# Kernel tuning notes

Hardware: AMD Instinct MI355X
Metric: run time of the kernel (lower is better)

Reference implementation:

```python
import jax, jax.numpy as jnp
import numpy as np

VOCAB, D_MODEL, N_EXPERTS, TOP_K = 32000, 768, 8, 2
D_FF = 4 * D_MODEL
BATCH, SEQ = 2, 2048


def setup_inputs() -> dict:
    key = jax.random.key(0)
    ks = jax.random.split(key, 6)
    s = 0.02
    return {
        "x": jax.random.randint(ks[0], (BATCH, SEQ), 0, VOCAB),
        "emb": jax.random.normal(ks[1], (VOCAB, D_MODEL), jnp.float32) * s,
        "gate_w": jax.random.normal(ks[2], (D_MODEL, N_EXPERTS), jnp.float32) * s,
        "gate_b": jnp.zeros((N_EXPERTS,), jnp.float32),
        "exp_w": jax.random.normal(ks[3], (N_EXPERTS, D_MODEL, D_FF), jnp.float32) * s,
        "exp_b": jnp.zeros((N_EXPERTS, D_FF), jnp.float32),
        "head_w": jax.random.normal(ks[4], (D_FF, VOCAB), jnp.float32) * s,
        "head_b": jnp.zeros((VOCAB,), jnp.float32),
    }


def reference(x, emb, gate_w, gate_b, exp_w, exp_b, head_w, head_b):
    B, S = x.shape
    h = emb[x]                                   # [B,S,D] embedding gather
    t = h.reshape(B * S, -1)                     # [T,D] token view
    logits = t @ gate_w + gate_b                 # [T,E] router
    topv, topi = jax.lax.top_k(logits, TOP_K)    # top-2 routing
    w = jax.nn.softmax(topv, axis=-1)            # renormalized gate weights
    T = t.shape[0]
    gates = jnp.zeros_like(logits).at[jnp.arange(T)[:, None], topi].set(w)  # [T,E]
    # expert FFN: Linear(d_model -> 4*d_model) + ReLU, dense over experts
    exp_out = jax.nn.relu(jnp.einsum('td,edf->tef', t, exp_w) + exp_b)      # [T,E,F]
    moe = jnp.einsum('te,tef->tf', gates, exp_out)                          # combine
    out = moe @ head_w + head_b                  # [T,V]
    return out.reshape(B, S, -1)
```

## Files before the change

### kernel.cpp

```cpp
#include <hip/hip_runtime.h>

typedef unsigned short u16;
typedef __attribute__((ext_vector_type(8))) short short8;
typedef __attribute__((ext_vector_type(4))) float f32x4;

#define T_TOKENS 4096
#define DMODEL   768
#define DFF      3072
#define NEXP     8
#define NVOCAB   32000

__device__ __forceinline__ u16 f2bf(float f) {
  unsigned u = __float_as_uint(f);
  u += 0x7FFFu + ((u >> 16) & 1u);
  return (u16)(u >> 16);
}
__device__ __forceinline__ float bf2f(u16 b) {
  return __uint_as_float(((unsigned)b) << 16);
}

__device__ __forceinline__ void async_load16(const void* g, void* lds) {
  __builtin_amdgcn_global_load_lds((const __attribute__((address_space(1))) void*)g,
                                   (__attribute__((address_space(3))) void*)lds, 16, 0, 0);
}

#define SBAR() __builtin_amdgcn_s_barrier()
#define VMCNT(n) asm volatile("s_waitcnt vmcnt(" #n ")")
#define SCHEDB() __builtin_amdgcn_sched_barrier(0)

__global__ __launch_bounds__(256) void k_embed_router(
    const int* __restrict__ x, const float* __restrict__ emb,
    const float* __restrict__ gw, const float* __restrict__ gb,
    u16* __restrict__ tbf, int* __restrict__ counts,
    int* __restrict__ tlist, float* __restrict__ wlist)
{
  __shared__ float partial[4][NEXP];
  const int t = blockIdx.x;
  const int tok = x[t];
  const float* er = emb + (size_t)tok * DMODEL;
  float p[NEXP];
#pragma unroll
  for (int e = 0; e < NEXP; ++e) p[e] = 0.f;
#pragma unroll
  for (int i = 0; i < 3; ++i) {
    const int d = threadIdx.x + i * 256;
    const float v = er[d];
    tbf[(size_t)t * DMODEL + d] = f2bf(v);
#pragma unroll
    for (int e = 0; e < NEXP; ++e) p[e] += v * gw[d * NEXP + e];
  }
#pragma unroll
  for (int e = 0; e < NEXP; ++e)
#pragma unroll
    for (int m = 32; m >= 1; m >>= 1) p[e] += __shfl_xor(p[e], m);
  const int lane = threadIdx.x & 63, wv = threadIdx.x >> 6;
  if (lane == 0)
    for (int e = 0; e < NEXP; ++e) partial[wv][e] = p[e];
  __syncthreads();
  if (threadIdx.x == 0) {
    float l[NEXP];
    for (int e = 0; e < NEXP; ++e)
      l[e] = partial[0][e] + partial[1][e] + partial[2][e] + partial[3][e] + gb[e];
    int i0 = 0;
    for (int e = 1; e < NEXP; ++e) if (l[e] > l[i0]) i0 = e;
    int i1 = -1;
    for (int e = 0; e < NEXP; ++e) { if (e == i0) continue; if (i1 < 0 || l[e] > l[i1]) i1 = e; }
    const float w0 = 1.f / (1.f + expf(l[i1] - l[i0]));
    int p0 = atomicAdd(&counts[0 * NEXP + i0], 1);
    tlist[(0 * NEXP + i0) * T_TOKENS + p0] = t;
    wlist[(0 * NEXP + i0) * T_TOKENS + p0] = w0;
    int p1 = atomicAdd(&counts[1 * NEXP + i1], 1);
    tlist[(1 * NEXP + i1) * T_TOKENS + p1] = t;
    wlist[(1 * NEXP + i1) * T_TOKENS + p1] = 1.f - w0;
  }
}

__global__ __launch_bounds__(256) void k_transpose_cvt(
    const float* __restrict__ src, u16* __restrict__ dst, int R, int C)
{
  __shared__ float tile[32][33];
  const float* s = src + (size_t)blockIdx.z * R * C;
  u16* d = dst + (size_t)blockIdx.z * R * C;
  const int tx = threadIdx.x & 31, ty = threadIdx.x >> 5;
  const int c = blockIdx.x * 32 + tx;
#pragma unroll
  for (int i = 0; i < 4; ++i) {
    const int r = blockIdx.y * 32 + ty + i * 8;
    tile[ty + i * 8][tx] = s[(size_t)r * C + c];
  }
  __syncthreads();
  const int rr = blockIdx.y * 32 + tx;
#pragma unroll
  for (int i = 0; i < 4; ++i) {
    const int cc = blockIdx.x * 32 + ty + i * 8;
    d[(size_t)cc * R + rr] = f2bf(tile[tx][ty + i * 8]);
  }
}

template <int SLOT1>
__global__ __launch_bounds__(256) void k_ffn_slot(
    const u16* __restrict__ tbf, const u16* __restrict__ BT,
    const float* __restrict__ eb, const int* __restrict__ counts,
    const int* __restrict__ tlist, const float* __restrict__ wlist,
    u16* __restrict__ moe)
{
  const int e = blockIdx.z;
  const int cnt = counts[SLOT1 * NEXP + e];
  const int mb = blockIdx.y;
  if (mb * 128 >= cnt) return;
  const int base = (SLOT1 * NEXP + e) * T_TOKENS + mb * 128;
  const int lim = cnt - mb * 128;

  __shared__ u16 aT[128 * 64];
  __shared__ u16 bT[128 * 64];
  const int tid = threadIdx.x;
  const int wave = tid >> 6, lane = tid & 63;
  const int wm = wave >> 1, wn = wave & 1;
  const int kg = lane >> 4, fr = lane & 15;
  const int n0 = blockIdx.x * 128;
  const u16* Be = BT + (size_t)e * DFF * DMODEL;

  int tokm[4];
#pragma unroll
  for (int it = 0; it < 4; ++it) {
    const int m = (it * 256 + tid) >> 3;
    tokm[it] = tlist[base + (m < lim ? m : lim - 1)];
  }

  f32x4 acc[4][4] = {};
  for (int ks = 0; ks < DMODEL / 64; ++ks) {
    __syncthreads();
    const int kb = ks * 64;
#pragma unroll
    for (int it = 0; it < 4; ++it) {
      const int c = it * 256 + tid;
      const int m = c >> 3;
      const int slot = (c & 7) ^ (m & 7);
      async_load16(tbf + (size_t)tokm[it] * DMODEL + kb + slot * 8,
                   &aT[(it * 256 + wave * 64) * 8]);
      async_load16(Be + (size_t)(n0 + m) * DMODEL + kb + slot * 8,
                   &bT[(it * 256 + wave * 64) * 8]);
    }
    __syncthreads();
#pragma unroll
    for (int kk = 0; kk < 2; ++kk) {
      short8 af[4], bf[4];
#pragma unroll
      for (int i = 0; i < 4; ++i) {
        const int am = wm * 64 + i * 16 + fr;
        const int kc = kk * 4 + kg;
        af[i] = *(const short8*)&aT[(am * 8 + (kc ^ (am & 7))) * 8];
        const int bn = wn * 64 + i * 16 + fr;
        bf[i] = *(const short8*)&bT[(bn * 8 + (kc ^ (bn & 7))) * 8];
      }
#pragma unroll
      for (int i = 0; i < 4; ++i)
#pragma unroll
        for (int j = 0; j < 4; ++j)
          acc[i][j] = __builtin_amdgcn_mfma_f32_16x16x32_bf16(af[i], bf[j], acc[i][j], 0, 0, 0);
    }
  }

  int trow[4][4]; float wrow[4][4];
#pragma unroll
  for (int i = 0; i < 4; ++i)
#pragma unroll
    for (int r = 0; r < 4; ++r) {
      const int row = wm * 64 + i * 16 + kg * 4 + r;
      if (row < lim) { trow[i][r] = tlist[base + row]; wrow[i][r] = wlist[base + row]; }
      else trow[i][r] = -1;
    }
#pragma unroll
  for (int j = 0; j < 4; ++j) {
    const int col = n0 + wn * 64 + j * 16 + fr;
    const float b = eb[e * DFF + col];
#pragma unroll
    for (int i = 0; i < 4; ++i)
#pragma unroll
      for (int r = 0; r < 4; ++r) {
        if (trow[i][r] < 0) continue;
        float v = acc[i][j][r] + b;
        v = v > 0.f ? v : 0.f;
        v *= wrow[i][r];
        u16* dst = &moe[(size_t)trow[i][r] * DFF + col];
        if (SLOT1) v += bf2f(*dst);
        *dst = f2bf(v);
      }
  }
}

__device__ __forceinline__ short8 frag(const u16* buf, int row, int kc) {
  return *(const short8*)(buf + (row * 8 + (kc ^ (row & 7))) * 8);
}

__global__ __launch_bounds__(512, 2) void k_head(
    const u16* __restrict__ A, const u16* __restrict__ BT,
    const float* __restrict__ bias, float* __restrict__ C)
{
  __shared__ u16 aL[2][256 * 64];
  __shared__ u16 bL[2][256 * 64];
  const int tid = threadIdx.x;
  const int lane = tid & 63, wave = tid >> 6;
  const int wm = wave >> 2, wn = wave & 3;
  const int kg = lane >> 4, fr = lane & 15;
  const int wg = (int)blockIdx.x;
  const int swz = (wg & 7) * 250 + (wg >> 3);
  const int m0 = (swz & 15) * 256;
  const int n0 = (swz >> 4) * 256;
  const int K = DFF, NT = K / 64;

  size_t gAo[2], gBo[2]; int lAo[2], lBo[2];
#pragma unroll
  for (int i = 0; i < 2; ++i) {
    const int c = i * 512 + tid, rl = c >> 3, s = c & 7;
    const int rA = (rl & 63) + ((rl >> 6) << 7);
    const int gsA = s ^ (rA & 7);
    gAo[i] = (size_t)(m0 + rA) * K + gsA * 8;
    lAo[i] = rA * 64 + s * 8;
    const int rB = (rl & 31) + ((rl >> 5) << 6);
    const int gsB = s ^ (rB & 7);
    gBo[i] = (size_t)(n0 + rB) * K + gsB * 8;
    lBo[i] = rB * 64 + s * 8;
  }
  auto stageA = [&](int kb, u16* buf, int h) {
#pragma unroll
    for (int i = 0; i < 2; ++i)
      async_load16(A + gAo[i] + (size_t)(h * 64) * K + kb, buf + lAo[i] + h * 4096);
  };
  auto stageB = [&](int kb, u16* buf, int h) {
#pragma unroll
    for (int i = 0; i < 2; ++i)
      async_load16(BT + gBo[i] + (size_t)(h * 32) * K + kb, buf + lBo[i] + h * 2048);
  };

  f32x4 acc[8][4] = {};
  short8 af[4][2], bfl[2][2], bfh[2][2];

  stageA(0, aL[0], 0); stageA(0, aL[0], 1);
  stageB(0, bL[0], 0); stageB(0, bL[0], 1);
  stageA(64, aL[1], 0); stageB(64, bL[1], 0); stageB(64, bL[1], 1);
  VMCNT(6);
  SCHEDB();
  SBAR();
#pragma unroll
  for (int mi = 0; mi < 4; ++mi)
#pragma unroll
    for (int kk = 0; kk < 2; ++kk)
      af[mi][kk] = frag(aL[0], wm * 128 + mi * 16 + fr, kk * 4 + kg);
#pragma unroll
  for (int ni = 0; ni < 2; ++ni)
#pragma unroll
    for (int kk = 0; kk < 2; ++kk) {
      bfl[ni][kk] = frag(bL[0], wn * 64 + ni * 16 + fr, kk * 4 + kg);
      bfh[ni][kk] = frag(bL[0], wn * 64 + 32 + ni * 16 + fr, kk * 4 + kg);
    }

  for (int t = 0; t < NT; ++t) {
    const int cur = t & 1;
    const u16* a_ = aL[cur];
    const u16* b_ = bL[cur];
    u16* aw = aL[cur];
    u16* bw = bL[cur];
    u16* an = aL[cur ^ 1];
    const u16* bn = bL[cur ^ 1];
    const int kb1 = (t + 1) * 64, kb2 = (t + 2) * 64;

    if (t + 1 < NT) stageA(kb1, an, 1);
    __builtin_amdgcn_s_setprio(1);
#pragma unroll
    for (int mi = 0; mi < 4; ++mi)
#pragma unroll
      for (int ni = 0; ni < 2; ++ni)
#pragma unroll
        for (int kk = 0; kk < 2; ++kk) {
          acc[mi][ni]     = __builtin_amdgcn_mfma_f32_16x16x32_bf16(af[mi][kk], bfl[ni][kk], acc[mi][ni], 0, 0, 0);
          acc[mi][ni + 2] = __builtin_amdgcn_mfma_f32_16x16x32_bf16(af[mi][kk], bfh[ni][kk], acc[mi][ni + 2], 0, 0, 0);
        }
    __builtin_amdgcn_s_setprio(0);
#pragma unroll
    for (int mi = 0; mi < 4; ++mi)
#pragma unroll
      for (int kk = 0; kk < 2; ++kk)
        af[mi][kk] = frag(a_, wm * 128 + 64 + mi * 16 + fr, kk * 4 + kg);
    if (t + 1 < NT) { VMCNT(2); SCHEDB(); }
    SBAR();

    if (t + 2 < NT) { stageA(kb2, aw, 0); stageB(kb2, bw, 0); stageB(kb2, bw, 1); }
    __builtin_amdgcn_s_setprio(1);
#pragma unroll
    for (int mi = 0; mi < 4; ++mi)
#pragma unroll
      for (int ni = 0; ni < 2; ++ni)
#pragma unroll
        for (int kk = 0; kk < 2; ++kk) {
          acc[mi + 4][ni]     = __builtin_amdgcn_mfma_f32_16x16x32_bf16(af[mi][kk], bfl[ni][kk], acc[mi + 4][ni], 0, 0, 0);
          acc[mi + 4][ni + 2] = __builtin_amdgcn_mfma_f32_16x16x32_bf16(af[mi][kk], bfh[ni][kk], acc[mi + 4][ni + 2], 0, 0, 0);
        }
    __builtin_amdgcn_s_setprio(0);
    if (t + 1 < NT) {
#pragma unroll
      for (int mi = 0; mi < 4; ++mi)
#pragma unroll
        for (int kk = 0; kk < 2; ++kk)
          af[mi][kk] = frag(an, wm * 128 + mi * 16 + fr, kk * 4 + kg);
#pragma unroll
      for (int ni = 0; ni < 2; ++ni)
#pragma unroll
        for (int kk = 0; kk < 2; ++kk) {
          bfl[ni][kk] = frag(bn, wn * 64 + ni * 16 + fr, kk * 4 + kg);
          bfh[ni][kk] = frag(bn, wn * 64 + 32 + ni * 16 + fr, kk * 4 + kg);
        }
      if (t + 2 < NT) { VMCNT(6); } else { VMCNT(0); }
      SCHEDB();
    }
    SBAR();
  }

#pragma unroll
  for (int ni = 0; ni < 4; ++ni) {
    const int col = n0 + wn * 64 + ni * 16 + fr;
    const float b = bias[col];
#pragma unroll
    for (int mi = 0; mi < 8; ++mi) {
      const int row = m0 + wm * 128 + (mi >> 2) * 64 + (mi & 3) * 16 + kg * 4;
#pragma unroll
      for (int r = 0; r < 4; ++r)
        __builtin_nontemporal_store(acc[mi][ni][r] + b,
                                    &C[(size_t)(row + r) * NVOCAB + col]);
    }
  }
}

extern "C" void kernel_launch(void* const* d_in, const int* in_sizes, int n_in,
                              void* d_out, int out_size, void* d_ws, size_t ws_size,
                              hipStream_t stream) {
  const int*   x     = (const int*)d_in[0];
  const float* emb   = (const float*)d_in[1];
  const float* gw    = (const float*)d_in[2];
  const float* gb    = (const float*)d_in[3];
  const float* expw  = (const float*)d_in[4];
  const float* expb  = (const float*)d_in[5];
  const float* headw = (const float*)d_in[6];
  const float* headb = (const float*)d_in[7];
  float* out = (float*)d_out;

  char* ws = (char*)d_ws;
  size_t off = 0;
  auto alloc = [&](size_t bytes) { size_t r = off; off += (bytes + 255) & ~(size_t)255; return r; };
  u16*   tbf    = (u16*)(ws + alloc((size_t)T_TOKENS * DMODEL * 2));
  int*   counts = (int*)(ws + alloc(2 * NEXP * 4));
  int*   tlist  = (int*)(ws + alloc((size_t)2 * NEXP * T_TOKENS * 4));
  float* wlist  = (float*)(ws + alloc((size_t)2 * NEXP * T_TOKENS * 4));
  u16*   expwT  = (u16*)(ws + alloc((size_t)NEXP * DFF * DMODEL * 2));
  u16*   headwT = (u16*)(ws + alloc((size_t)NVOCAB * DFF * 2));
  u16*   moe    = (u16*)(ws + alloc((size_t)T_TOKENS * DFF * 2));

  hipMemsetAsync(counts, 0, 2 * NEXP * 4, stream);
  k_embed_router<<<T_TOKENS, 256, 0, stream>>>(x, emb, gw, gb, tbf, counts, tlist, wlist);
  k_transpose_cvt<<<dim3(DFF / 32, DMODEL / 32, NEXP), 256, 0, stream>>>(expw, expwT, DMODEL, DFF);
  k_transpose_cvt<<<dim3(NVOCAB / 32, DFF / 32, 1), 256, 0, stream>>>(headw, headwT, DFF, NVOCAB);
  k_ffn_slot<0><<<dim3(DFF / 128, T_TOKENS / 128, NEXP), 256, 0, stream>>>(
      tbf, expwT, expb, counts, tlist, wlist, moe);
  k_ffn_slot<1><<<dim3(DFF / 128, T_TOKENS / 128, NEXP), 256, 0, stream>>>(
      tbf, expwT, expb, counts, tlist, wlist, moe);
  k_head<<<(T_TOKENS / 256) * (NVOCAB / 256), 512, 0, stream>>>(moe, headwT, headb, out);
}
```

Baseline: 1.181 ms.

## Double-buffer FFN expert GEMM with async prefetch and widen transpose tiles

The expert FFN kernel now double-buffers its LDS tiles and stages the next K-slices with async global-to-LDS loads while MFMAs run on the current slice. Fragment reads are split into halves and synchronisation is done with explicit vmcnt waits and barriers, replacing the two full syncthreads per K step. The weight transpose-convert kernel moves to 64x64 tiles and writes two bf16 values per 32-bit store. In exchange the FFN kernel uses twice the LDS and has a harder wait/barrier schedule to reason about.

Result: no change. 1.167 ms, median of 2 (-1.2%).

```diff
diff --git a/kernel.cpp b/kernel.cpp
--- a/kernel.cpp
+++ b/kernel.cpp
@@ -27,6 +27,10 @@
 #define SBAR() __builtin_amdgcn_s_barrier()
 #define VMCNT(n) asm volatile("s_waitcnt vmcnt(" #n ")")
 #define SCHEDB() __builtin_amdgcn_sched_barrier(0)
+
+__device__ __forceinline__ short8 frag(const u16* buf, int row, int kc) {
+  return *(const short8*)(buf + (row * 8 + (kc ^ (row & 7))) * 8);
+}
 
 __global__ __launch_bounds__(256) void k_embed_router(
     const int* __restrict__ x, const float* __restrict__ emb,
@@ -78,22 +82,26 @@
 __global__ __launch_bounds__(256) void k_transpose_cvt(
     const float* __restrict__ src, u16* __restrict__ dst, int R, int C)
 {
-  __shared__ float tile[32][33];
+  __shared__ float tile[64][65];
   const float* s = src + (size_t)blockIdx.z * R * C;
   u16* d = dst + (size_t)blockIdx.z * R * C;
-  const int tx = threadIdx.x & 31, ty = threadIdx.x >> 5;
-  const int c = blockIdx.x * 32 + tx;
-#pragma unroll
-  for (int i = 0; i < 4; ++i) {
-    const int r = blockIdx.y * 32 + ty + i * 8;
-    tile[ty + i * 8][tx] = s[(size_t)r * C + c];
+  const int tx = threadIdx.x & 63, ty = threadIdx.x >> 6;
+  const int c = blockIdx.x * 64 + tx;
+#pragma unroll
+  for (int i = 0; i < 16; ++i) {
+    const int r = blockIdx.y * 64 + ty + i * 4;
+    tile[ty + i * 4][tx] = s[(size_t)r * C + c];
   }
   __syncthreads();
-  const int rr = blockIdx.y * 32 + tx;
-#pragma unroll
-  for (int i = 0; i < 4; ++i) {
-    const int cc = blockIdx.x * 32 + ty + i * 8;
-    d[(size_t)cc * R + rr] = f2bf(tile[tx][ty + i * 8]);
+  const int h = threadIdx.x & 31, v = threadIdx.x >> 5;
+  const int rr = blockIdx.y * 64 + h * 2;
+#pragma unroll
+  for (int i = 0; i < 8; ++i) {
+    const int ccl = v + i * 8;
+    const int cc = blockIdx.x * 64 + ccl;
+    const unsigned lo = f2bf(tile[h * 2][ccl]);
+    const unsigned hi = f2bf(tile[h * 2 + 1][ccl]);
+    *(unsigned*)&d[(size_t)cc * R + rr] = lo | (hi << 16);
   }
 }
 
@@ -111,54 +119,109 @@
   const int base = (SLOT1 * NEXP + e) * T_TOKENS + mb * 128;
   const int lim = cnt - mb * 128;
 
-  __shared__ u16 aT[128 * 64];
-  __shared__ u16 bT[128 * 64];
+  __shared__ u16 aT[2][128 * 64];
+  __shared__ u16 bT[2][128 * 64];
   const int tid = threadIdx.x;
   const int wave = tid >> 6, lane = tid & 63;
   const int wm = wave >> 1, wn = wave & 1;
   const int kg = lane >> 4, fr = lane & 15;
   const int n0 = blockIdx.x * 128;
   const u16* Be = BT + (size_t)e * DFF * DMODEL;
-
-  int tokm[4];
-#pragma unroll
-  for (int it = 0; it < 4; ++it) {
-    const int m = (it * 256 + tid) >> 3;
-    tokm[it] = tlist[base + (m < lim ? m : lim - 1)];
-  }
+  const int K = DMODEL, NT = K / 64;
+
+  int gs8[2], lOf[2]; size_t gBo[2]; int tokA[2][2];
+#pragma unroll
+  for (int i = 0; i < 2; ++i) {
+    const int cch = i * 256 + tid, rl = cch >> 3, sft = cch & 7;
+    const int rb = (rl & 31) + ((rl >> 5) << 6);
+    gs8[i] = (sft ^ (rl & 7)) * 8;
+    lOf[i] = rb * 64 + sft * 8;
+    gBo[i] = (size_t)(n0 + rb) * K + gs8[i];
+#pragma unroll
+    for (int hh = 0; hh < 2; ++hh) {
+      const int row = rb + hh * 32;
+      tokA[i][hh] = tlist[base + (row < lim ? row : lim - 1)];
+    }
+  }
+  auto stageA = [&](int kb, u16* buf, int h) {
+#pragma unroll
+    for (int i = 0; i < 2; ++i)
+      async_load16(tbf + (size_t)tokA[i][h] * K + kb + gs8[i], buf + lOf[i] + h * 2048);
+  };
+  auto stageB = [&](int kb, u16* buf, int h) {
+#pragma unroll
+    for (int i = 0; i < 2; ++i)
+      async_load16(Be + gBo[i] + (size_t)(h * 32) * K + kb, buf + lOf[i] + h * 2048);
+  };
 
   f32x4 acc[4][4] = {};
-  for (int ks = 0; ks < DMODEL / 64; ++ks) {
-    __syncthreads();
-    const int kb = ks * 64;
-#pragma unroll
-    for (int it = 0; it < 4; ++it) {
-      const int c = it * 256 + tid;
-      const int m = c >> 3;
-      const int slot = (c & 7) ^ (m & 7);
-      async_load16(tbf + (size_t)tokm[it] * DMODEL + kb + slot * 8,
-                   &aT[(it * 256 + wave * 64) * 8]);
-      async_load16(Be + (size_t)(n0 + m) * DMODEL + kb + slot * 8,
-                   &bT[(it * 256 + wave * 64) * 8]);
-    }
-    __syncthreads();
-#pragma unroll
-    for (int kk = 0; kk < 2; ++kk) {
-      short8 af[4], bf[4];
-#pragma unroll
-      for (int i = 0; i < 4; ++i) {
-        const int am = wm * 64 + i * 16 + fr;
-        const int kc = kk * 4 + kg;
-        af[i] = *(const short8*)&aT[(am * 8 + (kc ^ (am & 7))) * 8];
-        const int bn = wn * 64 + i * 16 + fr;
-        bf[i] = *(const short8*)&bT[(bn * 8 + (kc ^ (bn & 7))) * 8];
-      }
-#pragma unroll
-      for (int i = 0; i < 4; ++i)
-#pragma unroll
-        for (int j = 0; j < 4; ++j)
-          acc[i][j] = __builtin_amdgcn_mfma_f32_16x16x32_bf16(af[i], bf[j], acc[i][j], 0, 0, 0);
-    }
+  short8 afA[2][2], afB[2][2], bf[4][2];
+
+  stageA(0, aT[0], 0); stageA(0, aT[0], 1);
+  stageB(0, bT[0], 0); stageB(0, bT[0], 1);
+  stageA(64, aT[1], 0); stageB(64, bT[1], 0); stageB(64, bT[1], 1);
+  VMCNT(6); SCHEDB(); SBAR();
+#pragma unroll
+  for (int i = 0; i < 2; ++i)
+#pragma unroll
+    for (int kk = 0; kk < 2; ++kk)
+      afA[i][kk] = frag(aT[0], wm * 64 + i * 16 + fr, kk * 4 + kg);
+#pragma unroll
+  for (int j = 0; j < 4; ++j)
+#pragma unroll
+    for (int kk = 0; kk < 2; ++kk)
+      bf[j][kk] = frag(bT[0], wn * 64 + j * 16 + fr, kk * 4 + kg);
+
+  for (int t = 0; t < NT; ++t) {
+    const int cur = t & 1;
+    const u16* a_ = aT[cur];
+    u16* aw = aT[cur]; u16* bw = bT[cur];
+    u16* an = aT[cur ^ 1]; const u16* bn = bT[cur ^ 1];
+    const int kb1 = (t + 1) * 64, kb2 = (t + 2) * 64;
+
+    if (t + 1 < NT) stageA(kb1, an, 1);
+    __builtin_amdgcn_s_setprio(1);
+#pragma unroll
+    for (int i = 0; i < 2; ++i)
+#pragma unroll
+      for (int j = 0; j < 4; ++j)
+#pragma unroll
+        for (int kk = 0; kk < 2; ++kk)
+          acc[i][j] = __builtin_amdgcn_mfma_f32_16x16x32_bf16(afA[i][kk], bf[j][kk], acc[i][j], 0, 0, 0);
+    __builtin_amdgcn_s_setprio(0);
+#pragma unroll
+    for (int i = 0; i < 2; ++i)
+#pragma unroll
+      for (int kk = 0; kk < 2; ++kk)
+        afB[i][kk] = frag(a_, wm * 64 + 32 + i * 16 + fr, kk * 4 + kg);
+    if (t + 1 < NT) { VMCNT(2); SCHEDB(); }
+    SBAR();
+
+    if (t + 2 < NT) { stageA(kb2, aw, 0); stageB(kb2, bw, 0); stageB(kb2, bw, 1); }
+    __builtin_amdgcn_s_setprio(1);
+#pragma unroll
+    for (int i = 0; i < 2; ++i)
+#pragma unroll
+      for (int j = 0; j < 4; ++j)
+#pragma unroll
+        for (int kk = 0; kk < 2; ++kk)
+          acc[i + 2][j] = __builtin_amdgcn_mfma_f32_16x16x32_bf16(afB[i][kk], bf[j][kk], acc[i + 2][j], 0, 0, 0);
+    __builtin_amdgcn_s_setprio(0);
+    if (t + 1 < NT) {
+#pragma unroll
+      for (int i = 0; i < 2; ++i)
+#pragma unroll
+        for (int kk = 0; kk < 2; ++kk)
+          afA[i][kk] = frag(an, wm * 64 + i * 16 + fr, kk * 4 + kg);
+#pragma unroll
+      for (int j = 0; j < 4; ++j)
+#pragma unroll
+        for (int kk = 0; kk < 2; ++kk)
+          bf[j][kk] = frag(bn, wn * 64 + j * 16 + fr, kk * 4 + kg);
+      if (t + 2 < NT) { VMCNT(6); } else { VMCNT(0); }
+      SCHEDB();
+    }
+    SBAR();
   }
 
   int trow[4][4]; float wrow[4][4];
@@ -187,10 +250,6 @@
         *dst = f2bf(v);
       }
   }
-}
-
-__device__ __forceinline__ short8 frag(const u16* buf, int row, int kc) {
-  return *(const short8*)(buf + (row * 8 + (kc ^ (row & 7))) * 8);
 }
 
 __global__ __launch_bounds__(512, 2) void k_head(
@@ -258,7 +317,6 @@
   for (int t = 0; t < NT; ++t) {
     const int cur = t & 1;
     const u16* a_ = aL[cur];
-    const u16* b_ = bL[cur];
     u16* aw = aL[cur];
     u16* bw = bL[cur];
     u16* an = aL[cur ^ 1];
@@ -357,8 +415,8 @@
 
   hipMemsetAsync(counts, 0, 2 * NEXP * 4, stream);
   k_embed_router<<<T_TOKENS, 256, 0, stream>>>(x, emb, gw, gb, tbf, counts, tlist, wlist);
-  k_transpose_cvt<<<dim3(DFF / 32, DMODEL / 32, NEXP), 256, 0, stream>>>(expw, expwT, DMODEL, DFF);
-  k_transpose_cvt<<<dim3(NVOCAB / 32, DFF / 32, 1), 256, 0, stream>>>(headw, headwT, DFF, NVOCAB);
+  k_transpose_cvt<<<dim3(DFF / 64, DMODEL / 64, NEXP), 256, 0, stream>>>(expw, expwT, DMODEL, DFF);
+  k_transpose_cvt<<<dim3(NVOCAB / 64, DFF / 64, 1), 256, 0, stream>>>(headw, headwT, DFF, NVOCAB);
   k_ffn_slot<0><<<dim3(DFF / 128, T_TOKENS / 128, NEXP), 256, 0, stream>>>(
       tbf, expwT, expb, counts, tlist, wlist, moe);
   k_ffn_slot<1><<<dim3(DFF / 128, T_TOKENS / 128, NEXP), 256, 0, stream>>>(
```
